# Kernel tuning notes

Measured on AMD Instinct MI355X. Metric: run time of the kernel, lower is better.

## Reference

```python
import jax, jax.numpy as jnp
import numpy as np

NMAX = 8
LMAX = 3
RC = 5.0
SIGMA = 0.5
SMOOTH_W = 0.5
N_SPECIES = 4
N_ATOMS = 20000
N_EDGES = 800000
LMMAX = (LMAX + 1) ** 2  # 16
# map each (l,m) flat index to its l (block structure of mult_ln_lm)
LM_TO_L = jnp.asarray(np.repeat(np.arange(LMAX + 1), 2 * np.arange(LMAX + 1) + 1))


def real_sph_harm_l3(d):
    """Real spherical harmonics, integral normalization, l=0..3. d: [J,3] unit vectors."""
    x, y, z = d[:, 0], d[:, 1], d[:, 2]
    x2, y2, z2 = x * x, y * y, z * z
    cols = [
        jnp.full_like(x, 0.28209479177387814),                 # l=0
        0.4886025119029199 * y,                                # l=1, m=-1
        0.4886025119029199 * z,                                # l=1, m=0
        0.4886025119029199 * x,                                # l=1, m=1
        1.0925484305920792 * x * y,                            # l=2, m=-2
        1.0925484305920792 * y * z,                            # l=2, m=-1
        0.31539156525252005 * (2.0 * z2 - x2 - y2),            # l=2, m=0
        1.0925484305920792 * x * z,                            # l=2, m=1
        0.5462742152960396 * (x2 - y2),                        # l=2, m=2
        0.5900435899266435 * y * (3.0 * x2 - y2),              # l=3, m=-3
        2.890611442640554 * x * y * z,                         # l=3, m=-2
        0.4570457994644658 * y * (4.0 * z2 - x2 - y2),         # l=3, m=-1
        0.3731763325901154 * z * (2.0 * z2 - 3.0 * x2 - 3.0 * y2),  # l=3, m=0
        0.4570457994644658 * x * (4.0 * z2 - x2 - y2),         # l=3, m=1
        1.445305721320277 * z * (x2 - y2),                     # l=3, m=2
        0.5900435899266435 * x * (x2 - 3.0 * y2),              # l=3, m=3
    ]
    return jnp.stack(cols, axis=-1)  # [J, 16]


def shifted_cosine_cutoff(r):
    """f=1 for r<rc-w, smooth cosine decay to 0 at rc, 0 beyond."""
    w = SMOOTH_W
    t = 0.5 * (1.0 + jnp.cos(jnp.pi * jnp.clip((r - (RC - w)) / w, 0.0, 1.0)))
    return jnp.where(r < RC - w, 1.0, jnp.where(r < RC, t, 0.0))


def setup_inputs() -> dict:
    key = jax.random.key(0)
    k1, k2, k3, k4, k5, k6 = jax.random.split(key, 6)
    distances = jax.random.uniform(k1, (N_EDGES,), jnp.float32, 0.05, RC * 0.999)
    dv = jax.random.normal(k2, (N_EDGES, 3), jnp.float32)
    direction_vectors = dv / jnp.linalg.norm(dv, axis=1, keepdims=True)
    radial_centers = jax.random.uniform(k3, ((LMAX + 1) * NMAX,), jnp.float32, 0.0, RC)
    z = jax.random.randint(k4, (N_ATOMS,), 0, N_SPECIES)
    idx_i = jax.random.randint(k5, (N_EDGES,), 0, N_ATOMS)
    idx_j = jax.random.randint(k6, (N_EDGES,), 0, N_ATOMS)
    return {"distances": distances, "direction_vectors": direction_vectors,
            "radial_centers": radial_centers, "z": z, "idx_i": idx_i, "idx_j": idx_j}


def reference(distances, direction_vectors, radial_centers, z, idx_i, idx_j):
    J = distances.shape[0]
    # spherical harmonics of edge directions: [J, lmmax]
    Ylm = real_sph_harm_l3(direction_vectors)
    # radial integrals (Gaussian-basis spline surrogate) * cutoff: [J, lmax+1, nmax]
    rb = jnp.exp(-0.5 * jnp.square((distances[:, None] - radial_centers[None, :]) / SIGMA))
    RIln = rb.reshape(J, LMAX + 1, NMAX) * shifted_cosine_cutoff(distances)[:, None, None]
    # block-wise outer product (vectorized mult_ln_lm): [J, nmax, lmmax]
    cij_nlm = RIln[:, LM_TO_L, :].transpose(0, 2, 1) * Ylm[:, None, :]
    # species- and atom-dependent scatter-add
    reduction_ids = z[idx_j] + N_SPECIES * idx_i
    ci = jax.ops.segment_sum(cij_nlm.reshape(J, -1), reduction_ids,
                             num_segments=N_SPECIES * N_ATOMS)
    return ci.reshape(N_ATOMS, N_SPECIES, NMAX, LMMAX)
```

## Files before the change

kernel.cpp:

```cpp
#include <hip/hip_runtime.h>
#include <math.h>


#define NSPEC 4
#define CAP   32

typedef float v2f __attribute__((ext_vector_type(2)));

__constant__ float YCOEF[16 * 20] = {
    0.28209479177387814f,0,0,0, 0,0,0,0, 0,0,0,0, 0,0,0,0, 0,0,0,0,
    0,0,0.4886025119029199f,0, 0,0,0,0, 0,0,0,0, 0,0,0,0, 0,0,0,0,
    0,0,0,0.4886025119029199f, 0,0,0,0, 0,0,0,0, 0,0,0,0, 0,0,0,0,
    0,0.4886025119029199f,0,0, 0,0,0,0, 0,0,0,0, 0,0,0,0, 0,0,0,0,
    0,0,0,0, 0,0,0,1.0925484305920792f, 0,0,0,0, 0,0,0,0, 0,0,0,0,
    0,0,0,0, 0,0,0,0, 0,1.0925484305920792f,0,0, 0,0,0,0, 0,0,0,0,
    0,0,0,0, -0.31539156525252005f,-0.31539156525252005f,0.6307831305050401f,0, 0,0,0,0, 0,0,0,0, 0,0,0,0,
    0,0,0,0, 0,0,0,0, 1.0925484305920792f,0,0,0, 0,0,0,0, 0,0,0,0,
    0,0,0,0, 0.5462742152960396f,-0.5462742152960396f,0,0, 0,0,0,0, 0,0,0,0, 0,0,0,0,
    0,0,0,0, 0,0,0,0, 0,0,0,1.7701307697799305f, 0,0,0,0, -0.5900435899266435f,0,0,0,
    0,0,0,0, 0,0,0,0, 0,0,0,0, 0,0,2.890611442640554f,0, 0,0,0,0,
    0,0,0,0, 0,0,0,0, 0,0,0,-0.4570457994644658f, 0,0,0,0, -0.4570457994644658f,0,1.8281831978578632f,0,
    0,0,0,0, 0,0,0,0, 0,0,0,0, -1.1195289977703462f,0,0,0, 0,-1.1195289977703462f,0,0.7463526651802308f,
    0,0,0,0, 0,0,0,0, 0,0,-0.4570457994644658f,0, 0,-0.4570457994644658f,0,1.8281831978578632f, 0,0,0,0,
    0,0,0,0, 0,0,0,0, 0,0,0,0, 1.445305721320277f,0,0,0, 0,-1.445305721320277f,0,0,
    0,0,0,0, 0,0,0,0, 0,0,0.5900435899266435f,0, 0,-1.7701307697799305f,0,0, 0,0,0,0,
};

__device__ __forceinline__ void gather_row(
    const float2* __restrict__ payload, const float* __restrict__ dirs,
    const float* __restrict__ centers, float* __restrict__ out,
    int row, int lane, int beg, int end)
{
    int q = lane >> 4;
    int t = lane & 15;
    int l = (t >= 9) ? 3 : (t >= 4) ? 2 : (t >= 1) ? 1 : 0;
    float cenA = centers[2 * t];
    float cenB = centers[2 * t + 1];
    int srcA = (q << 4) + (l << 2);

    const float4* cr = (const float4*)(&YCOEF[t * 20]);
    float4 c0 = cr[0], c1 = cr[1], c2 = cr[2], c3 = cr[3], c4 = cr[4];
    v2f K0 = {c0.x, c0.y}, K1 = {c0.z, c0.w};
    v2f K2 = {c1.x, c1.y}, K3 = {c1.z, c1.w};
    v2f K4 = {c2.x, c2.y}, K5 = {c2.z, c2.w};
    v2f K6 = {c3.x, c3.y}, K7 = {c3.z, c3.w};
    v2f K8 = {c4.x, c4.y}, K9 = {c4.z, c4.w};
    asm volatile("" : "+v"(K0), "+v"(K1), "+v"(K2), "+v"(K3), "+v"(K4),
                      "+v"(K5), "+v"(K6), "+v"(K7), "+v"(K8), "+v"(K9),
                      "+v"(cenA), "+v"(cenB));

    v2f A0 = {0, 0}, A1 = {0, 0}, A2 = {0, 0}, A3 = {0, 0};

    int cnt = end - beg;
    if (cnt > 0) {
        int last = end - 1;
        int slot = beg + q;
        int c0s = slot < end ? slot : last;
        int c1s = slot + 4 < end ? slot + 4 : last;
        float2 B0 = payload[c0s];
        float2 B1 = payload[c1s];
        int e0 = __float_as_int(B0.x);
        float x  = dirs[3 * e0 + 0];
        float y  = dirs[3 * e0 + 1];
        float zc = dirs[3 * e0 + 2];
        int iters = (cnt + 3) >> 2;
        for (int it = 0; it < iters; ++it) {
            int s2 = slot + 8;
            float2 B2 = payload[s2 < end ? s2 : last];
            int e1 = __float_as_int(B1.x);
            float xn = dirs[3 * e1 + 0];
            float yn = dirs[3 * e1 + 1];
            float zn = dirs[3 * e1 + 2];

            bool v = slot < end;
            float xm = v ? x    : 0.0f;
            float ym = v ? y    : 0.0f;
            float zm = v ? zc   : 0.0f;
            float rm = v ? B0.y : 10.0f;

            float dA = rm - cenA;
            float dB = rm - cenB;
            float rb0 = __expf(-2.0f * dA * dA);
            float rb1 = __expf(-2.0f * dB * dB);

            float b0 = __shfl(rb0, srcA,     64);
            float b1 = __shfl(rb1, srcA,     64);
            float b2 = __shfl(rb0, srcA + 1, 64);
            float b3 = __shfl(rb1, srcA + 1, 64);
            float b4 = __shfl(rb0, srcA + 2, 64);
            float b5 = __shfl(rb1, srcA + 2, 64);
            float b6 = __shfl(rb0, srcA + 3, 64);
            float b7 = __shfl(rb1, srcA + 3, 64);

            float xx = xm * xm, yy = ym * ym, zz = zm * zm;
            v2f m0 = {1.0f, xm};
            v2f m1 = {ym, zm};
            v2f m2 = {xx, yy};
            v2f m3 = {zz, xm * ym};
            v2f m4 = {xm * zm, ym * zm};
            v2f m5 = {xx * xm, xx * ym};
            v2f m6 = {xx * zm, xm * yy};
            v2f m7 = {xm * ym * zm, xm * zz};
            v2f m8 = {yy * ym, yy * zm};
            v2f m9 = {ym * zz, zz * zm};

            v2f pa = K0 * m0 + K1 * m1;
            v2f pb = K2 * m2 + K3 * m3;
            pa += K4 * m4;
            pb += K5 * m5;
            pa += K6 * m6;
            pb += K7 * m7;
            pa += K8 * m8;
            pb += K9 * m9;
            v2f ps = pa + pb;
            float ylm = ps.x + ps.y;

            float u  = fminf(fmaxf((rm - 4.5f) * 2.0f, 0.0f), 1.0f);
            float fc = fmaf(0.5f, __cosf(3.14159265358979f * u), 0.5f);
            float p  = fc * ylm;

            v2f pp = {p, p};
            A0 += pp * (v2f){b0, b1};
            A1 += pp * (v2f){b2, b3};
            A2 += pp * (v2f){b4, b5};
            A3 += pp * (v2f){b6, b7};

            B0 = B1; B1 = B2;
            x = xn; y = yn; zc = zn;
            slot += 4;
        }
    }

    A0.x += __shfl_xor(A0.x, 16, 64); A0.x += __shfl_xor(A0.x, 32, 64);
    A0.y += __shfl_xor(A0.y, 16, 64); A0.y += __shfl_xor(A0.y, 32, 64);
    A1.x += __shfl_xor(A1.x, 16, 64); A1.x += __shfl_xor(A1.x, 32, 64);
    A1.y += __shfl_xor(A1.y, 16, 64); A1.y += __shfl_xor(A1.y, 32, 64);
    A2.x += __shfl_xor(A2.x, 16, 64); A2.x += __shfl_xor(A2.x, 32, 64);
    A2.y += __shfl_xor(A2.y, 16, 64); A2.y += __shfl_xor(A2.y, 32, 64);
    A3.x += __shfl_xor(A3.x, 16, 64); A3.x += __shfl_xor(A3.x, 32, 64);
    A3.y += __shfl_xor(A3.y, 16, 64); A3.y += __shfl_xor(A3.y, 32, 64);

    float w0, w1;
    switch (q) {
        case 0: w0 = A0.x; w1 = A0.y; break;
        case 1: w0 = A1.x; w1 = A1.y; break;
        case 2: w0 = A2.x; w1 = A2.y; break;
        default: w0 = A3.x; w1 = A3.y; break;
    }
    float* o = out + (size_t)row * 128;
    o[32 * q + t]      = w0;
    o[32 * q + 16 + t] = w1;
}

__global__ __launch_bounds__(256) void k_scatter_direct(
    const float* __restrict__ dist,
    const int* __restrict__ zsp, const int* __restrict__ idx_i,
    const int* __restrict__ idx_j,
    int* __restrict__ cnt, float2* __restrict__ payload, int J)
{
    int e = blockIdx.x * 256 + threadIdx.x;
    if (e >= J) return;
    int rid = zsp[idx_j[e]] + NSPEC * idx_i[e];
    float r = dist[e];
    int pos = atomicAdd(&cnt[rid], 1);
    if (pos < CAP) {
        float2 v;
        v.x = __int_as_float(e);
        v.y = r;
        payload[rid * CAP + pos] = v;
    }
}

__global__ __launch_bounds__(256) void k_gather_big(
    const float2* __restrict__ payload, const float* __restrict__ dirs,
    const float* __restrict__ centers,
    const int* __restrict__ cnt, float* __restrict__ out, int nrows)
{
    int wave = threadIdx.x >> 6;
    int lane = threadIdx.x & 63;
    int row = blockIdx.x * 4 + wave;
    if (row >= nrows) return;
    int c = cnt[row];
    c = c < CAP ? c : CAP;
    int beg = row * CAP;
    gather_row(payload, dirs, centers, out, row, lane, beg, beg + c);
}

__global__ __launch_bounds__(256) void k_hist(
    const int* __restrict__ zsp, const int* __restrict__ idx_i,
    const int* __restrict__ idx_j, int* __restrict__ counts, int J)
{
    int e = blockIdx.x * 256 + threadIdx.x;
    if (e >= J) return;
    atomicAdd(&counts[zsp[idx_j[e]] + NSPEC * idx_i[e]], 1);
}

__global__ __launch_bounds__(256) void k_scan1(
    const int* __restrict__ counts, int* __restrict__ cursor,
    int* __restrict__ bsums, int n)
{
    __shared__ int s[256];
    int i = blockIdx.x * 256 + threadIdx.x;
    int v = (i < n) ? counts[i] : 0;
    s[threadIdx.x] = v;
    __syncthreads();
    for (int off = 1; off < 256; off <<= 1) {
        int t = (threadIdx.x >= off) ? s[threadIdx.x - off] : 0;
        __syncthreads();
        s[threadIdx.x] += t;
        __syncthreads();
    }
    if (i < n) cursor[i] = s[threadIdx.x] - v;
    if (threadIdx.x == 255) bsums[blockIdx.x] = s[255];
}

__global__ __launch_bounds__(512) void k_scan2(int* __restrict__ bsums, int nb)
{
    __shared__ int s[512];
    int t = threadIdx.x;
    int v = (t < nb) ? bsums[t] : 0;
    s[t] = v;
    __syncthreads();
    for (int off = 1; off < 512; off <<= 1) {
        int u = (t >= off) ? s[t - off] : 0;
        __syncthreads();
        s[t] += u;
        __syncthreads();
    }
    if (t < nb) bsums[t] = s[t] - v;
}

__global__ __launch_bounds__(256) void k_scatter(
    const float* __restrict__ dist,
    const int* __restrict__ zsp, const int* __restrict__ idx_i,
    const int* __restrict__ idx_j,
    int* __restrict__ cursor, const int* __restrict__ bsums,
    float2* __restrict__ payload, int J)
{
    int e = blockIdx.x * 256 + threadIdx.x;
    if (e >= J) return;
    int rid = zsp[idx_j[e]] + NSPEC * idx_i[e];
    int pos = bsums[rid >> 8] + atomicAdd(&cursor[rid], 1);
    float2 v;
    v.x = __int_as_float(e);
    v.y = dist[e];
    payload[pos] = v;
}

__global__ __launch_bounds__(256) void k_gather_small(
    const float2* __restrict__ payload, const float* __restrict__ dirs,
    const float* __restrict__ centers,
    const int* __restrict__ cursor, const int* __restrict__ bsums,
    float* __restrict__ out, int nrows)
{
    int wave = threadIdx.x >> 6;
    int lane = threadIdx.x & 63;
    int row = blockIdx.x * 4 + wave;
    if (row >= nrows) return;
    int end = bsums[row >> 8] + cursor[row];
    int beg = (row == 0) ? 0 : bsums[(row - 1) >> 8] + cursor[row - 1];
    gather_row(payload, dirs, centers, out, row, lane, beg, end);
}

__global__ __launch_bounds__(256) void sphexp16_fb(
    const float* __restrict__ dist, const float* __restrict__ dirs,
    const float* __restrict__ centers, const int* __restrict__ zsp,
    const int* __restrict__ idx_i, const int* __restrict__ idx_j,
    float* __restrict__ out, int J)
{
    int tid = blockIdx.x * 256 + threadIdx.x;
    int e = tid >> 4, t = tid & 15;
    if (e >= J) return;
    float r = dist[e];
    float x = dirs[3*e], y = dirs[3*e+1], z = dirs[3*e+2];
    int rid = zsp[idx_j[e]] + NSPEC * idx_i[e];
    size_t base = (size_t)rid * 128 + t;
    const float* cr = &YCOEF[t * 20];
    float xx=x*x, yy=y*y, zz=z*z;
    float ylm = cr[0] + cr[1]*x + cr[2]*y + cr[3]*z
              + cr[4]*xx + cr[5]*yy + cr[6]*zz + cr[7]*(x*y)
              + cr[8]*(x*z) + cr[9]*(y*z)
              + cr[10]*(xx*x) + cr[11]*(xx*y) + cr[12]*(xx*z)
              + cr[13]*(x*yy) + cr[14]*(x*y*z) + cr[15]*(x*zz)
              + cr[16]*(yy*y) + cr[17]*(yy*z) + cr[18]*(y*zz) + cr[19]*(zz*z);
    float u = fminf(fmaxf((r - 4.5f) * 2.0f, 0.0f), 1.0f);
    float fc = 0.5f * (1.0f + __cosf(3.14159265358979f * u));
    int l = (t >= 9) ? 3 : (t >= 4) ? 2 : (t >= 1) ? 1 : 0;
    float pref = fc * ylm;
#pragma unroll
    for (int n = 0; n < 8; n++) {
        float d = r - centers[l*8+n];
        atomicAdd(out + base + (size_t)(n*16), pref * __expf(-2.0f*d*d));
    }
}

extern "C" void kernel_launch(void* const* d_in, const int* in_sizes, int n_in,
                              void* d_out, int out_size, void* d_ws, size_t ws_size,
                              hipStream_t stream) {
    const float* dist    = (const float*)d_in[0];
    const float* dirs    = (const float*)d_in[1];
    const float* centers = (const float*)d_in[2];
    const int*   zsp     = (const int*)d_in[3];
    const int*   idx_i   = (const int*)d_in[4];
    const int*   idx_j   = (const int*)d_in[5];
    float* out = (float*)d_out;

    int J      = in_sizes[0];
    int natoms = in_sizes[3];
    int nrows  = natoms * NSPEC;
    int nb1    = (nrows + 255) / 256;

    size_t need_big   = (size_t)nrows * CAP * 8 + (size_t)nrows * 4;
    size_t need_small = (size_t)J * 8 + (2 * (size_t)nrows + 512) * 4;

    if (ws_size >= need_big) {
        float2* payload = (float2*)d_ws;
        int* cnt = (int*)(payload + (size_t)nrows * CAP);
        hipMemsetAsync(cnt, 0, (size_t)nrows * sizeof(int), stream);
        k_scatter_direct<<<(J + 255) / 256, 256, 0, stream>>>(
            dist, zsp, idx_i, idx_j, cnt, payload, J);
        k_gather_big<<<(nrows + 3) / 4, 256, 0, stream>>>(
            payload, dirs, centers, cnt, out, nrows);
    } else if (ws_size >= need_small && nb1 <= 512) {
        float2* payload = (float2*)d_ws;
        int* counts = (int*)(payload + J);
        int* cursor = counts + nrows;
        int* bsums  = cursor + nrows;
        hipMemsetAsync(counts, 0, (size_t)nrows * sizeof(int), stream);
        k_hist<<<(J + 255) / 256, 256, 0, stream>>>(zsp, idx_i, idx_j, counts, J);
        k_scan1<<<nb1, 256, 0, stream>>>(counts, cursor, bsums, nrows);
        k_scan2<<<1, 512, 0, stream>>>(bsums, nb1);
        k_scatter<<<(J + 255) / 256, 256, 0, stream>>>(
            dist, zsp, idx_i, idx_j, cursor, bsums, payload, J);
        k_gather_small<<<(nrows + 3) / 4, 256, 0, stream>>>(
            payload, dirs, centers, cursor, bsums, out, nrows);
    } else {
        hipMemsetAsync(d_out, 0, (size_t)out_size * sizeof(float), stream);
        long long total = (long long)J * 16;
        sphexp16_fb<<<(int)((total + 255) / 256), 256, 0, stream>>>(
            dist, dirs, centers, zsp, idx_i, idx_j, out, J);
    }
}
```

Before: 176.3 us.

## Pack direction x,y and signed radius into scatter payload, recompute z

The scatter kernels now write each edge's x, y direction components plus the distance into the bucketed payload. The sign of z is stored in the distance's low mantissa bit. The gather kernel reconstructs z as sqrt(1-x²-y²) with that sign, which removes the dependent indirect load of direction vectors through the edge index. This trades 12-byte uncoalesced payload records and a sqrt per edge for fewer random gathers, and it adds precision loss in z near the equator and a one-ulp perturbation of r.

```diff
diff --git a/kernel.cpp b/kernel.cpp
--- a/kernel.cpp
+++ b/kernel.cpp
@@ -27,9 +27,8 @@
 };
 
 __device__ __forceinline__ void gather_row(
-    const float2* __restrict__ payload, const float* __restrict__ dirs,
-    const float* __restrict__ centers, float* __restrict__ out,
-    int row, int lane, int beg, int end)
+    const float* __restrict__ pay, const float* __restrict__ centers,
+    float* __restrict__ out, int row, int lane, int beg, int end)
 {
     int q = lane >> 4;
     int t = lane & 15;
@@ -55,28 +54,25 @@
     if (cnt > 0) {
         int last = end - 1;
         int slot = beg + q;
-        int c0s = slot < end ? slot : last;
-        int c1s = slot + 4 < end ? slot + 4 : last;
-        float2 B0 = payload[c0s];
-        float2 B1 = payload[c1s];
-        int e0 = __float_as_int(B0.x);
-        float x  = dirs[3 * e0 + 0];
-        float y  = dirs[3 * e0 + 1];
-        float zc = dirs[3 * e0 + 2];
+        int s0 = slot     < end ? slot     : last;
+        int s1 = slot + 4 < end ? slot + 4 : last;
+        const float* p0 = pay + 3 * (size_t)s0;
+        const float* p1 = pay + 3 * (size_t)s1;
+        float B0x = p0[0], B0y = p0[1], B0r = p0[2];
+        float B1x = p1[0], B1y = p1[1], B1r = p1[2];
         int iters = (cnt + 3) >> 2;
         for (int it = 0; it < iters; ++it) {
             int s2 = slot + 8;
-            float2 B2 = payload[s2 < end ? s2 : last];
-            int e1 = __float_as_int(B1.x);
-            float xn = dirs[3 * e1 + 0];
-            float yn = dirs[3 * e1 + 1];
-            float zn = dirs[3 * e1 + 2];
-
-            bool v = slot < end;
-            float xm = v ? x    : 0.0f;
-            float ym = v ? y    : 0.0f;
-            float zm = v ? zc   : 0.0f;
-            float rm = v ? B0.y : 10.0f;
+            s2 = s2 < end ? s2 : last;
+            const float* p2 = pay + 3 * (size_t)s2;
+            float B2x = p2[0], B2y = p2[1], B2r = p2[2];
+
+            float xm = B0x, ym = B0y;
+            int   ri = __float_as_int(B0r);
+            float rm = B0r;
+            float zz0 = fmaxf(fmaf(-xm, xm, fmaf(-ym, ym, 1.0f)), 0.0f);
+            float zm = sqrtf(zz0);
+            zm = (ri & 1) ? -zm : zm;
 
             float dA = rm - cenA;
             float dB = rm - cenB;
@@ -92,17 +88,17 @@
             float b6 = __shfl(rb0, srcA + 3, 64);
             float b7 = __shfl(rb1, srcA + 3, 64);
 
-            float xx = xm * xm, yy = ym * ym, zz = zm * zm;
+            float xx = xm * xm, yy = ym * ym, zzq = zm * zm;
             v2f m0 = {1.0f, xm};
             v2f m1 = {ym, zm};
             v2f m2 = {xx, yy};
-            v2f m3 = {zz, xm * ym};
+            v2f m3 = {zzq, xm * ym};
             v2f m4 = {xm * zm, ym * zm};
             v2f m5 = {xx * xm, xx * ym};
             v2f m6 = {xx * zm, xm * yy};
-            v2f m7 = {xm * ym * zm, xm * zz};
+            v2f m7 = {xm * ym * zm, xm * zzq};
             v2f m8 = {yy * ym, yy * zm};
-            v2f m9 = {ym * zz, zz * zm};
+            v2f m9 = {ym * zzq, zzq * zm};
 
             v2f pa = K0 * m0 + K1 * m1;
             v2f pb = K2 * m2 + K3 * m3;
@@ -118,6 +114,7 @@
             float u  = fminf(fmaxf((rm - 4.5f) * 2.0f, 0.0f), 1.0f);
             float fc = fmaf(0.5f, __cosf(3.14159265358979f * u), 0.5f);
             float p  = fc * ylm;
+            p = (slot < end) ? p : 0.0f;
 
             v2f pp = {p, p};
             A0 += pp * (v2f){b0, b1};
@@ -125,8 +122,8 @@
             A2 += pp * (v2f){b4, b5};
             A3 += pp * (v2f){b6, b7};
 
-            B0 = B1; B1 = B2;
-            x = xn; y = yn; zc = zn;
+            B0x = B1x; B0y = B1y; B0r = B1r;
+            B1x = B2x; B1y = B2y; B1r = B2r;
             slot += 4;
         }
     }
@@ -153,27 +150,28 @@
 }
 
 __global__ __launch_bounds__(256) void k_scatter_direct(
-    const float* __restrict__ dist,
+    const float* __restrict__ dist, const float* __restrict__ dirs,
     const int* __restrict__ zsp, const int* __restrict__ idx_i,
     const int* __restrict__ idx_j,
-    int* __restrict__ cnt, float2* __restrict__ payload, int J)
+    int* __restrict__ cnt, float* __restrict__ pay, int J)
 {
     int e = blockIdx.x * 256 + threadIdx.x;
     if (e >= J) return;
     int rid = zsp[idx_j[e]] + NSPEC * idx_i[e];
     float r = dist[e];
+    float x = dirs[3 * e + 0];
+    float y = dirs[3 * e + 1];
+    float z = dirs[3 * e + 2];
+    int rs = (__float_as_int(r) & ~1) | (z < 0.0f ? 1 : 0);
     int pos = atomicAdd(&cnt[rid], 1);
     if (pos < CAP) {
-        float2 v;
-        v.x = __int_as_float(e);
-        v.y = r;
-        payload[rid * CAP + pos] = v;
+        float* p = pay + 3 * ((size_t)rid * CAP + pos);
+        p[0] = x; p[1] = y; p[2] = __int_as_float(rs);
     }
 }
 
 __global__ __launch_bounds__(256) void k_gather_big(
-    const float2* __restrict__ payload, const float* __restrict__ dirs,
-    const float* __restrict__ centers,
+    const float* __restrict__ pay, const float* __restrict__ centers,
     const int* __restrict__ cnt, float* __restrict__ out, int nrows)
 {
     int wave = threadIdx.x >> 6;
@@ -183,7 +181,7 @@
     int c = cnt[row];
     c = c < CAP ? c : CAP;
     int beg = row * CAP;
-    gather_row(payload, dirs, centers, out, row, lane, beg, beg + c);
+    gather_row(pay, centers, out, row, lane, beg, beg + c);
 }
 
 __global__ __launch_bounds__(256) void k_hist(
@@ -231,25 +229,27 @@
 }
 
 __global__ __launch_bounds__(256) void k_scatter(
-    const float* __restrict__ dist,
+    const float* __restrict__ dist, const float* __restrict__ dirs,
     const int* __restrict__ zsp, const int* __restrict__ idx_i,
     const int* __restrict__ idx_j,
     int* __restrict__ cursor, const int* __restrict__ bsums,
-    float2* __restrict__ payload, int J)
+    float* __restrict__ pay, int J)
 {
     int e = blockIdx.x * 256 + threadIdx.x;
     if (e >= J) return;
     int rid = zsp[idx_j[e]] + NSPEC * idx_i[e];
+    float r = dist[e];
+    float x = dirs[3 * e + 0];
+    float y = dirs[3 * e + 1];
+    float z = dirs[3 * e + 2];
+    int rs = (__float_as_int(r) & ~1) | (z < 0.0f ? 1 : 0);
     int pos = bsums[rid >> 8] + atomicAdd(&cursor[rid], 1);
-    float2 v;
-    v.x = __int_as_float(e);
-    v.y = dist[e];
-    payload[pos] = v;
+    float* p = pay + 3 * (size_t)pos;
+    p[0] = x; p[1] = y; p[2] = __int_as_float(rs);
 }
 
 __global__ __launch_bounds__(256) void k_gather_small(
-    const float2* __restrict__ payload, const float* __restrict__ dirs,
-    const float* __restrict__ centers,
+    const float* __restrict__ pay, const float* __restrict__ centers,
     const int* __restrict__ cursor, const int* __restrict__ bsums,
     float* __restrict__ out, int nrows)
 {
@@ -259,7 +259,7 @@
     if (row >= nrows) return;
     int end = bsums[row >> 8] + cursor[row];
     int beg = (row == 0) ? 0 : bsums[(row - 1) >> 8] + cursor[row - 1];
-    gather_row(payload, dirs, centers, out, row, lane, beg, end);
+    gather_row(pay, centers, out, row, lane, beg, end);
 }
 
 __global__ __launch_bounds__(256) void sphexp16_fb(
@@ -310,20 +310,20 @@
     int nrows  = natoms * NSPEC;
     int nb1    = (nrows + 255) / 256;
 
-    size_t need_big   = (size_t)nrows * CAP * 8 + (size_t)nrows * 4;
-    size_t need_small = (size_t)J * 8 + (2 * (size_t)nrows + 512) * 4;
+    size_t need_big   = (size_t)nrows * CAP * 12 + (size_t)nrows * 4;
+    size_t need_small = (size_t)J * 12 + (2 * (size_t)nrows + 512) * 4;
 
     if (ws_size >= need_big) {
-        float2* payload = (float2*)d_ws;
-        int* cnt = (int*)(payload + (size_t)nrows * CAP);
+        float* pay = (float*)d_ws;
+        int* cnt = (int*)(pay + 3 * (size_t)nrows * CAP);
         hipMemsetAsync(cnt, 0, (size_t)nrows * sizeof(int), stream);
         k_scatter_direct<<<(J + 255) / 256, 256, 0, stream>>>(
-            dist, zsp, idx_i, idx_j, cnt, payload, J);
+            dist, dirs, zsp, idx_i, idx_j, cnt, pay, J);
         k_gather_big<<<(nrows + 3) / 4, 256, 0, stream>>>(
-            payload, dirs, centers, cnt, out, nrows);
+            pay, centers, cnt, out, nrows);
     } else if (ws_size >= need_small && nb1 <= 512) {
-        float2* payload = (float2*)d_ws;
-        int* counts = (int*)(payload + J);
+        float* pay = (float*)d_ws;
+        int* counts = (int*)(pay + 3 * (size_t)J);
         int* cursor = counts + nrows;
         int* bsums  = cursor + nrows;
         hipMemsetAsync(counts, 0, (size_t)nrows * sizeof(int), stream);
@@ -331,9 +331,9 @@
         k_scan1<<<nb1, 256, 0, stream>>>(counts, cursor, bsums, nrows);
         k_scan2<<<1, 512, 0, stream>>>(bsums, nb1);
         k_scatter<<<(J + 255) / 256, 256, 0, stream>>>(
-            dist, zsp, idx_i, idx_j, cursor, bsums, payload, J);
+            dist, dirs, zsp, idx_i, idx_j, cursor, bsums, pay, J);
         k_gather_small<<<(nrows + 3) / 4, 256, 0, stream>>>(
-            payload, dirs, centers, cursor, bsums, out, nrows);
+            pay, centers, cursor, bsums, out, nrows);
     } else {
         hipMemsetAsync(d_out, 0, (size_t)out_size * sizeof(float), stream);
         long long total = (long long)J * 16;
```

Result: no change. 176.3 us (-0.0%).
